# Performance work log

Measured on AMD Instinct MI355X. Metric: run time of the kernel, lower is better.

## Reference

```python
import jax, jax.numpy as jnp
import numpy as np

BETA = 0.5  # hard-negative concentration (module default)


def _l2norm(x, axis):
    return x / jnp.linalg.norm(x, axis=axis, keepdims=True)


def setup_inputs() -> dict:
    key = jax.random.key(0)
    k1, k2, k3 = jax.random.split(key, 3)
    B, V, D = 4096, 2, 512
    features = jax.random.normal(k1, (B, V, D), dtype=jnp.float32)
    out_1 = jax.random.normal(k2, (B, D), dtype=jnp.float32)
    out_2 = jax.random.normal(k3, (B, D), dtype=jnp.float32)
    indexes = jnp.arange(B, dtype=jnp.int64)
    return {"features": features, "out_1": out_1, "out_2": out_2, "indexes": indexes}


def reference(features, out_1, out_2, indexes):
    # features is normalized in the original forward but unused afterwards
    _ = _l2norm(features, axis=2)

    o1 = _l2norm(out_1, axis=-1)
    o2 = _l2norm(out_2, axis=-1)
    out = jnp.concatenate([o1, o2], axis=0)            # [2B, D]
    label = jnp.concatenate([indexes, indexes], axis=0)  # [2B]
    batch = label.shape[0]

    # cost = exp(2 * out @ out.T), [2B, 2B]
    cost = jnp.exp(2.0 * jnp.einsum('id,jd->ij', out, out))

    pos_full = (label[:, None] == label[None, :]).astype(cost.dtype)
    neg_index = 1.0 - pos_full
    pos_index = pos_full - jnp.eye(batch, dtype=cost.dtype)

    pos = pos_index * cost
    neg = neg_index * cost

    # importance weights: neg_index * exp(beta * log(neg)) == neg_index * neg**beta
    imp = jax.lax.stop_gradient(neg_index * jnp.power(neg, BETA))
    neg_exp_sum = (imp * neg).sum(axis=-1) / imp.sum(axis=-1)  # [2B]

    denom = pos + (batch - 2) * neg_exp_sum[:, None]
    ratio = pos / denom

    mask = pos_index > 0
    safe_ratio = jnp.where(mask, ratio, 1.0)
    nce = -(jnp.log(safe_ratio) * pos_index).sum() / pos_index.sum()
    return nce
```

## Files before the change

### kernel.cpp

```cpp
#include <hip/hip_runtime.h>
#include <stdint.h>

#define BHALF 4096
#define NROWS 8192
#define DDIM  512
#define KNEG  8190.0f

#define BM   128
#define BK   32
#define NTIL 64
#define TBLK (NTIL * (NTIL + 1) / 2)
#define RBLK 32

typedef short v8s __attribute__((ext_vector_type(8)));
typedef float v4f __attribute__((ext_vector_type(4)));

static __device__ inline float bf2f(uint32_t u) {
    union { uint32_t i; float f; } c; c.i = u << 16; return c.f;
}
static __device__ inline uint32_t f2bf(float f) {
    union { float f; uint32_t i; } c; c.f = f;
    return (c.i + 0x7fffu + ((c.i >> 16) & 1u)) >> 16;
}

#define GLL16(gp, lp)                                                         \
    __builtin_amdgcn_global_load_lds(                                         \
        (__attribute__((address_space(1))) void*)(gp),                        \
        (__attribute__((address_space(3))) void*)(lp), 16, 0, 0)

__global__ __launch_bounds__(256) void rownorm_cvt_kernel(
    const void* __restrict__ o1, const void* __restrict__ o2,
    float* __restrict__ rn, uint16_t* __restrict__ cvt)
{
    int wave = threadIdx.x >> 6, lane = threadIdx.x & 63;
    int row = blockIdx.x * 4 + wave;

    uint32_t w = ((const uint32_t*)o1)[lane * 977 + 13];
    uint32_t e = (w >> 7) & 0xFFu;
    int bad = (e < 100u || e > 140u) ? 1 : 0;
    #pragma unroll
    for (int m = 32; m; m >>= 1) bad += __shfl_xor(bad, m);

    float ss;
    uint4 pack;
    if (bad <= 16) {
        const uint16_t* s = (row < BHALF)
            ? (const uint16_t*)o1 + (size_t)row * DDIM
            : (const uint16_t*)o2 + (size_t)(row - BHALF) * DDIM;
        pack = ((const uint4*)s)[lane];
        float a0 = bf2f(pack.x & 0xffffu), a1 = bf2f(pack.x >> 16);
        float a2 = bf2f(pack.y & 0xffffu), a3 = bf2f(pack.y >> 16);
        float a4 = bf2f(pack.z & 0xffffu), a5 = bf2f(pack.z >> 16);
        float a6 = bf2f(pack.w & 0xffffu), a7 = bf2f(pack.w >> 16);
        ss = a0*a0 + a1*a1 + a2*a2 + a3*a3 + a4*a4 + a5*a5 + a6*a6 + a7*a7;
    } else {
        const float* s = (row < BHALF)
            ? (const float*)o1 + (size_t)row * DDIM
            : (const float*)o2 + (size_t)(row - BHALF) * DDIM;
        float4 a = ((const float4*)s)[2 * lane];
        float4 b = ((const float4*)s)[2 * lane + 1];
        ss = a.x*a.x + a.y*a.y + a.z*a.z + a.w*a.w
           + b.x*b.x + b.y*b.y + b.z*b.z + b.w*b.w;
        pack.x = f2bf(a.x) | (f2bf(a.y) << 16);
        pack.y = f2bf(a.z) | (f2bf(a.w) << 16);
        pack.z = f2bf(b.x) | (f2bf(b.y) << 16);
        pack.w = f2bf(b.z) | (f2bf(b.w) << 16);
    }
    *(uint4*)(cvt + (size_t)row * DDIM + lane * 8) = pack;

    #pragma unroll
    for (int m = 32; m; m >>= 1) ss += __shfl_xor(ss, m);
    if (lane == 0) rn[row] = rsqrtf(ss);
}

__global__ __launch_bounds__(256, 4) void SupCon_hcl_49323404427556_kernel(
    const uint16_t* __restrict__ cvt, const float* __restrict__ rn,
    float* __restrict__ pden, float* __restrict__ pnum, float* __restrict__ cpos)
{
    __shared__ alignas(16) uint16_t la[BM * BK];
    __shared__ alignas(16) uint16_t lb[BM * BK];
    __shared__ float rnA[BM], rnB[BM];
    __shared__ float s_dr[BM][2], s_nr[BM][2], s_dc[BM][2], s_nc[BM][2];

    int tid  = threadIdx.x;
    int wave = tid >> 6, lane = tid & 63;
    int quad = lane >> 4, l16 = lane & 15;
    int wrow = (wave >> 1) * 64, wcol = (wave & 1) * 64;

    int t = blockIdx.x;
    int bi = (int)(64.5f - sqrtf(64.5f * 64.5f - 2.0f * (float)t));
    while (bi > 0 && (64 * bi - (bi * (bi - 1)) / 2) > t) --bi;
    while ((64 * (bi + 1) - ((bi + 1) * bi) / 2) <= t) ++bi;
    int bj = bi + (t - (64 * bi - (bi * (bi - 1)) / 2));
    int i0 = bi * BM, j0 = bj * BM;
    bool diag = (bi == bj);

    if (tid < BM) rnA[tid] = rn[i0 + tid];
    else          rnB[tid - BM] = rn[j0 + (tid - BM)];

    const uint16_t* A16 = cvt + (size_t)i0 * DDIM;
    const uint16_t* B16 = cvt + (size_t)j0 * DDIM;

    v4f acc[4][4];
    v4f z = {0.f, 0.f, 0.f, 0.f};
    #pragma unroll
    for (int a = 0; a < 4; ++a)
        #pragma unroll
        for (int b = 0; b < 4; ++b) acc[a][b] = z;

    int rloc = lane >> 2;
    int slot = lane & 3;
    int rA   = 32 * wave + rloc;
    int chk  = (slot - (rA >> 1)) & 3;
    const uint16_t* gA = A16 + (size_t)rA * DDIM + chk * 8;
    const uint16_t* gB = B16 + (size_t)rA * DDIM + chk * 8;
    uint16_t* sA0 = &la[(32 * wave) * BK];
    uint16_t* sA1 = &la[(32 * wave + 16) * BK];
    uint16_t* sB0 = &lb[(32 * wave) * BK];
    uint16_t* sB1 = &lb[(32 * wave + 16) * BK];

    const uint16_t* lbp = diag ? la : lb;
    int sfrag = (quad + (l16 >> 1)) & 3;

    for (int kb = 0; kb < DDIM / BK; ++kb) {
        __syncthreads();
        GLL16(gA + kb * BK, sA0);
        GLL16(gA + kb * BK + 16 * DDIM, sA1);
        if (!diag) {
            GLL16(gB + kb * BK, sB0);
            GLL16(gB + kb * BK + 16 * DDIM, sB1);
        }
        __syncthreads();

        v8s af[4], bfr[4];
        #pragma unroll
        for (int tt = 0; tt < 4; ++tt) {
            af[tt]  = *(const v8s*)(&la [(wrow + 16 * tt + l16) * BK + sfrag * 8]);
            bfr[tt] = *(const v8s*)(&lbp[(wcol + 16 * tt + l16) * BK + sfrag * 8]);
        }
        #pragma unroll
        for (int mt = 0; mt < 4; ++mt)
            #pragma unroll
            for (int nt = 0; nt < 4; ++nt)
                acc[mt][nt] = __builtin_amdgcn_mfma_f32_16x16x32_bf16(
                    af[mt], bfr[nt], acc[mt][nt], 0, 0, 0);
    }

    #pragma unroll
    for (int mt = 0; mt < 4; ++mt) {
        #pragma unroll
        for (int nt = 0; nt < 4; ++nt) {
            float rj = rnB[wcol + 16 * nt + l16];
            #pragma unroll
            for (int r = 0; r < 4; ++r) {
                float ri = rnA[wrow + 16 * mt + quad * 4 + r];
                acc[mt][nt][r] = __expf(acc[mt][nt][r] * ri * rj);
            }
        }
    }

    #pragma unroll
    for (int mt = 0; mt < 4; ++mt) {
        #pragma unroll
        for (int r = 0; r < 4; ++r) {
            int gil = wrow + 16 * mt + quad * 4 + r;
            int gi = i0 + gil;
            int partner = gi ^ BHALF;
            float pd = 0.f, pn = 0.f;
            #pragma unroll
            for (int nt = 0; nt < 4; ++nt) {
                int gj = j0 + wcol + 16 * nt + l16;
                float e = acc[mt][nt][r];
                if (gj == partner) cpos[gi] = e * e;
                if (gj != gi && gj != partner) { pd += e; pn += e * e * e; }
            }
            #pragma unroll
            for (int m = 1; m < 16; m <<= 1) {
                pd += __shfl_xor(pd, m);
                pn += __shfl_xor(pn, m);
            }
            if (l16 == 0) { s_dr[gil][wcol >> 6] = pd; s_nr[gil][wcol >> 6] = pn; }
        }
    }

    if (!diag) {
        #pragma unroll
        for (int nt = 0; nt < 4; ++nt) {
            int gjl = wcol + 16 * nt + l16;
            int gj = j0 + gjl;
            int pj = gj ^ BHALF;
            float cd = 0.f, cn = 0.f;
            #pragma unroll
            for (int mt = 0; mt < 4; ++mt) {
                #pragma unroll
                for (int r = 0; r < 4; ++r) {
                    int gi = i0 + wrow + 16 * mt + quad * 4 + r;
                    float e = acc[mt][nt][r];
                    if (gi == pj) cpos[gj] = e * e;
                    else { cd += e; cn += e * e * e; }
                }
            }
            cd += __shfl_xor(cd, 16); cn += __shfl_xor(cn, 16);
            cd += __shfl_xor(cd, 32); cn += __shfl_xor(cn, 32);
            if (quad == 0) { s_dc[gjl][wrow >> 6] = cd; s_nc[gjl][wrow >> 6] = cn; }
        }
    }

    __syncthreads();
    if (tid < BM) {
        pden[(size_t)bj * NROWS + i0 + tid] = s_dr[tid][0] + s_dr[tid][1];
        pnum[(size_t)bj * NROWS + i0 + tid] = s_nr[tid][0] + s_nr[tid][1];
        if (!diag) {
            pden[(size_t)bi * NROWS + j0 + tid] = s_dc[tid][0] + s_dc[tid][1];
            pnum[(size_t)bi * NROWS + j0 + tid] = s_nc[tid][0] + s_nc[tid][1];
        }
    }
}

__global__ __launch_bounds__(256) void finalizeA_kernel(
    const float* __restrict__ pden, const float* __restrict__ pnum,
    const float* __restrict__ cpos, float* __restrict__ bpart)
{
    int i = blockIdx.x * 256 + threadIdx.x;
    float den = 0.f, num = 0.f;
    #pragma unroll 8
    for (int x = 0; x < NTIL; ++x) {
        den += pden[(size_t)x * NROWS + i];
        num += pnum[(size_t)x * NROWS + i];
    }
    float s = logf(1.0f + KNEG * (num / den) / cpos[i]);
    for (int m = 32; m; m >>= 1) s += __shfl_xor(s, m);
    __shared__ float wsum[4];
    if ((threadIdx.x & 63) == 0) wsum[threadIdx.x >> 6] = s;
    __syncthreads();
    if (threadIdx.x == 0)
        bpart[blockIdx.x] = wsum[0] + wsum[1] + wsum[2] + wsum[3];
}

__global__ void finalizeB_kernel(const float* __restrict__ bpart, float* __restrict__ out)
{
    int lane = threadIdx.x;
    float s = (lane < RBLK) ? bpart[lane] : 0.f;
    for (int m = 32; m; m >>= 1) s += __shfl_xor(s, m);
    if (lane == 0) out[0] = s / (float)NROWS;
}

extern "C" void kernel_launch(void* const* d_in, const int* in_sizes, int n_in,
                              void* d_out, int out_size, void* d_ws, size_t ws_size,
                              hipStream_t stream)
{
    const void* o1 = d_in[1];
    const void* o2 = d_in[2];

    uint16_t* cvt = (uint16_t*)d_ws;
    float* pden = (float*)(cvt + (size_t)NROWS * DDIM);
    float* pnum = pden + (size_t)NTIL * NROWS;
    float* rn   = pnum + (size_t)NTIL * NROWS;
    float* cpos = rn + NROWS;
    float* bpart= cpos + NROWS;

    rownorm_cvt_kernel<<<NROWS / 4, 256, 0, stream>>>(o1, o2, rn, cvt);
    SupCon_hcl_49323404427556_kernel<<<TBLK, 256, 0, stream>>>(cvt, rn, pden, pnum, cpos);
    finalizeA_kernel<<<RBLK, 256, 0, stream>>>(pden, pnum, cpos, bpart);
    finalizeB_kernel<<<1, 64, 0, stream>>>(bpart, (float*)d_out);
}
```

Baseline: 152.4 us.

## Add fast epilogue for off-diagonal tiles and widen finalize reduction

Tiles that contain neither the diagonal nor the positive-partner entries now take a branch-free epilogue. It fuses the exp with the row and column accumulations, then reduces row sums with a butterfly transpose-reduce instead of per-row shuffle trees. The finalize step is split across 256 blocks with a two-level reduction over the 64 partial columns instead of 32 serial-loop blocks. Launch bounds drop to 3 waves per SIMD to leave room for the extra registers, which may lower occupancy.

```diff
diff --git a/kernel.cpp b/kernel.cpp
--- a/kernel.cpp
+++ b/kernel.cpp
@@ -10,7 +10,7 @@
 #define BK   32
 #define NTIL 64
 #define TBLK (NTIL * (NTIL + 1) / 2)
-#define RBLK 32
+#define FABLK 256
 
 typedef short v8s __attribute__((ext_vector_type(8)));
 typedef float v4f __attribute__((ext_vector_type(4)));
@@ -73,7 +73,7 @@
     if (lane == 0) rn[row] = rsqrtf(ss);
 }
 
-__global__ __launch_bounds__(256, 4) void SupCon_hcl_49323404427556_kernel(
+__global__ __launch_bounds__(256, 3) void SupCon_hcl_49323404427556_kernel(
     const uint16_t* __restrict__ cvt, const float* __restrict__ rn,
     float* __restrict__ pden, float* __restrict__ pnum, float* __restrict__ cpos)
 {
@@ -94,6 +94,8 @@
     int bj = bi + (t - (64 * bi - (bi * (bi - 1)) / 2));
     int i0 = bi * BM, j0 = bj * BM;
     bool diag = (bi == bj);
+    bool partner = (bj == bi + 32) && (bi < 32);
+    bool plain = !diag && !partner;
 
     if (tid < BM) rnA[tid] = rn[i0 + tid];
     else          rnB[tid - BM] = rn[j0 + (tid - BM)];
@@ -146,63 +148,117 @@
                     af[mt], bfr[nt], acc[mt][nt], 0, 0, 0);
     }
 
-    #pragma unroll
-    for (int mt = 0; mt < 4; ++mt) {
-        #pragma unroll
-        for (int nt = 0; nt < 4; ++nt) {
-            float rj = rnB[wcol + 16 * nt + l16];
+    if (plain) {
+        float rjv[4];
+        #pragma unroll
+        for (int nt = 0; nt < 4; ++nt) rjv[nt] = rnB[wcol + 16 * nt + l16];
+
+        float pd[16], pn[16], cdv[4], cnv[4];
+        #pragma unroll
+        for (int k = 0; k < 16; ++k) { pd[k] = 0.f; pn[k] = 0.f; }
+        #pragma unroll
+        for (int nt = 0; nt < 4; ++nt) { cdv[nt] = 0.f; cnv[nt] = 0.f; }
+
+        #pragma unroll
+        for (int mt = 0; mt < 4; ++mt) {
             #pragma unroll
             for (int r = 0; r < 4; ++r) {
                 float ri = rnA[wrow + 16 * mt + quad * 4 + r];
-                acc[mt][nt][r] = __expf(acc[mt][nt][r] * ri * rj);
-            }
-        }
-    }
-
-    #pragma unroll
-    for (int mt = 0; mt < 4; ++mt) {
-        #pragma unroll
-        for (int r = 0; r < 4; ++r) {
-            int gil = wrow + 16 * mt + quad * 4 + r;
-            int gi = i0 + gil;
-            int partner = gi ^ BHALF;
-            float pd = 0.f, pn = 0.f;
+                #pragma unroll
+                for (int nt = 0; nt < 4; ++nt) {
+                    float e  = __expf(acc[mt][nt][r] * ri * rjv[nt]);
+                    float e3 = e * e * e;
+                    pd[mt * 4 + r] += e;   pn[mt * 4 + r] += e3;
+                    cdv[nt]        += e;   cnv[nt]        += e3;
+                }
+            }
+        }
+
+        #define BSTEP(arr, n, bit)                                            \
+            _Pragma("unroll")                                                 \
+            for (int p = 0; p < (n); ++p) {                                   \
+                float mine = (l16 & (bit)) ? arr[2*p+1] : arr[2*p];           \
+                float send = (l16 & (bit)) ? arr[2*p]   : arr[2*p+1];         \
+                arr[p] = mine + __shfl_xor(send, (bit));                      \
+            }
+        BSTEP(pd, 8, 1) BSTEP(pd, 4, 2) BSTEP(pd, 2, 4) BSTEP(pd, 1, 8)
+        BSTEP(pn, 8, 1) BSTEP(pn, 4, 2) BSTEP(pn, 2, 4) BSTEP(pn, 1, 8)
+        #undef BSTEP
+
+        int rowk = wrow + 16 * (l16 >> 2) + quad * 4 + (l16 & 3);
+        s_dr[rowk][wcol >> 6] = pd[0];
+        s_nr[rowk][wcol >> 6] = pn[0];
+
+        #pragma unroll
+        for (int nt = 0; nt < 4; ++nt) {
+            float cd = cdv[nt] + __shfl_xor(cdv[nt], 16);
+            cd += __shfl_xor(cd, 32);
+            float cn = cnv[nt] + __shfl_xor(cnv[nt], 16);
+            cn += __shfl_xor(cn, 32);
+            if (quad == 0) {
+                s_dc[wcol + 16 * nt + l16][wrow >> 6] = cd;
+                s_nc[wcol + 16 * nt + l16][wrow >> 6] = cn;
+            }
+        }
+    } else {
+        #pragma unroll
+        for (int mt = 0; mt < 4; ++mt) {
             #pragma unroll
             for (int nt = 0; nt < 4; ++nt) {
-                int gj = j0 + wcol + 16 * nt + l16;
-                float e = acc[mt][nt][r];
-                if (gj == partner) cpos[gi] = e * e;
-                if (gj != gi && gj != partner) { pd += e; pn += e * e * e; }
-            }
-            #pragma unroll
-            for (int m = 1; m < 16; m <<= 1) {
-                pd += __shfl_xor(pd, m);
-                pn += __shfl_xor(pn, m);
-            }
-            if (l16 == 0) { s_dr[gil][wcol >> 6] = pd; s_nr[gil][wcol >> 6] = pn; }
-        }
-    }
-
-    if (!diag) {
-        #pragma unroll
-        for (int nt = 0; nt < 4; ++nt) {
-            int gjl = wcol + 16 * nt + l16;
-            int gj = j0 + gjl;
-            int pj = gj ^ BHALF;
-            float cd = 0.f, cn = 0.f;
-            #pragma unroll
-            for (int mt = 0; mt < 4; ++mt) {
+                float rj = rnB[wcol + 16 * nt + l16];
                 #pragma unroll
                 for (int r = 0; r < 4; ++r) {
-                    int gi = i0 + wrow + 16 * mt + quad * 4 + r;
+                    float ri = rnA[wrow + 16 * mt + quad * 4 + r];
+                    acc[mt][nt][r] = __expf(acc[mt][nt][r] * ri * rj);
+                }
+            }
+        }
+
+        #pragma unroll
+        for (int mt = 0; mt < 4; ++mt) {
+            #pragma unroll
+            for (int r = 0; r < 4; ++r) {
+                int gil = wrow + 16 * mt + quad * 4 + r;
+                int gi = i0 + gil;
+                int pr = gi ^ BHALF;
+                float pdv = 0.f, pnv = 0.f;
+                #pragma unroll
+                for (int nt = 0; nt < 4; ++nt) {
+                    int gj = j0 + wcol + 16 * nt + l16;
                     float e = acc[mt][nt][r];
-                    if (gi == pj) cpos[gj] = e * e;
-                    else { cd += e; cn += e * e * e; }
-                }
-            }
-            cd += __shfl_xor(cd, 16); cn += __shfl_xor(cn, 16);
-            cd += __shfl_xor(cd, 32); cn += __shfl_xor(cn, 32);
-            if (quad == 0) { s_dc[gjl][wrow >> 6] = cd; s_nc[gjl][wrow >> 6] = cn; }
+                    if (gj == pr) cpos[gi] = e * e;
+                    if (gj != gi && gj != pr) { pdv += e; pnv += e * e * e; }
+                }
+                #pragma unroll
+                for (int m = 1; m < 16; m <<= 1) {
+                    pdv += __shfl_xor(pdv, m);
+                    pnv += __shfl_xor(pnv, m);
+                }
+                if (l16 == 0) { s_dr[gil][wcol >> 6] = pdv; s_nr[gil][wcol >> 6] = pnv; }
+            }
+        }
+
+        if (!diag) {
+            #pragma unroll
+            for (int nt = 0; nt < 4; ++nt) {
+                int gjl = wcol + 16 * nt + l16;
+                int gj = j0 + gjl;
+                int pj = gj ^ BHALF;
+                float cd = 0.f, cn = 0.f;
+                #pragma unroll
+                for (int mt = 0; mt < 4; ++mt) {
+                    #pragma unroll
+                    for (int r = 0; r < 4; ++r) {
+                        int gi = i0 + wrow + 16 * mt + quad * 4 + r;
+                        float e = acc[mt][nt][r];
+                        if (gi == pj) cpos[gj] = e * e;
+                        else { cd += e; cn += e * e * e; }
+                    }
+                }
+                cd += __shfl_xor(cd, 16); cn += __shfl_xor(cn, 16);
+                cd += __shfl_xor(cd, 32); cn += __shfl_xor(cn, 32);
+                if (quad == 0) { s_dc[gjl][wrow >> 6] = cd; s_nc[gjl][wrow >> 6] = cn; }
+            }
         }
     }
 
@@ -221,28 +277,48 @@
     const float* __restrict__ pden, const float* __restrict__ pnum,
     const float* __restrict__ cpos, float* __restrict__ bpart)
 {
-    int i = blockIdx.x * 256 + threadIdx.x;
-    float den = 0.f, num = 0.f;
-    #pragma unroll 8
-    for (int x = 0; x < NTIL; ++x) {
-        den += pden[(size_t)x * NROWS + i];
-        num += pnum[(size_t)x * NROWS + i];
-    }
-    float s = logf(1.0f + KNEG * (num / den) / cpos[i]);
+    int b = blockIdx.x, t = threadIdx.x;
+    int r = b * 32 + (t & 31);
+    int c = t >> 5;
+    float pd = 0.f, pn = 0.f;
+    #pragma unroll
+    for (int i = 0; i < 8; ++i) {
+        int x = c + 8 * i;
+        pd += pden[(size_t)x * NROWS + r];
+        pn += pnum[(size_t)x * NROWS + r];
+    }
+    pd += __shfl_xor(pd, 32);
+    pn += __shfl_xor(pn, 32);
+
+    __shared__ float sd[4][32], sn[4][32];
+    int wave = t >> 6, lane = t & 63;
+    if (lane < 32) { sd[wave][lane] = pd; sn[wave][lane] = pn; }
+    __syncthreads();
+
+    float s = 0.f;
+    if (t < 32) {
+        float d = sd[0][t] + sd[1][t] + sd[2][t] + sd[3][t];
+        float n = sn[0][t] + sn[1][t] + sn[2][t] + sn[3][t];
+        s = logf(1.0f + KNEG * (n / d) / cpos[b * 32 + t]);
+    }
+    if (t < 64) {
+        #pragma unroll
+        for (int m = 32; m; m >>= 1) s += __shfl_xor(s, m);
+        if (t == 0) bpart[b] = s;
+    }
+}
+
+__global__ __launch_bounds__(256) void finalizeB_kernel(
+    const float* __restrict__ bpart, float* __restrict__ out)
+{
+    int t = threadIdx.x;
+    float s = bpart[t];
+    #pragma unroll
     for (int m = 32; m; m >>= 1) s += __shfl_xor(s, m);
     __shared__ float wsum[4];
-    if ((threadIdx.x & 63) == 0) wsum[threadIdx.x >> 6] = s;
+    if ((t & 63) == 0) wsum[t >> 6] = s;
     __syncthreads();
-    if (threadIdx.x == 0)
-        bpart[blockIdx.x] = wsum[0] + wsum[1] + wsum[2] + wsum[3];
-}
-
-__global__ void finalizeB_kernel(const float* __restrict__ bpart, float* __restrict__ out)
-{
-    int lane = threadIdx.x;
-    float s = (lane < RBLK) ? bpart[lane] : 0.f;
-    for (int m = 32; m; m >>= 1) s += __shfl_xor(s, m);
-    if (lane == 0) out[0] = s / (float)NROWS;
+    if (t == 0) out[0] = (wsum[0] + wsum[1] + wsum[2] + wsum[3]) / (float)NROWS;
 }
 
 extern "C" void kernel_launch(void* const* d_in, const int* in_sizes, int n_in,
@@ -261,6 +337,6 @@
 
     rownorm_cvt_kernel<<<NROWS / 4, 256, 0, stream>>>(o1, o2, rn, cvt);
     SupCon_hcl_49323404427556_kernel<<<TBLK, 256, 0, stream>>>(cvt, rn, pden, pnum, cpos);
-    finalizeA_kernel<<<RBLK, 256, 0, stream>>>(pden, pnum, cpos, bpart);
-    finalizeB_kernel<<<1, 64, 0, stream>>>(bpart, (float*)d_out);
-}
+    finalizeA_kernel<<<FABLK, 256, 0, stream>>>(pden, pnum, cpos, bpart);
+    finalizeB_kernel<<<1, 256, 0, stream>>>(bpart, (float*)d_out);
+}
```

After: 135.3 us. -11.2%, faster.
